# Performance work log

Measured on AMD Instinct MI355X. Metric: run time of the kernel, lower is better.

Reference implementation:

```python
import jax, jax.numpy as jnp
import numpy as np

E = 1024      # emb_size == hidden_size
H = 8         # n_heads
BATCH = 8
NUM = 48      # table rows
KW = 48       # table columns (keys)
L = NUM * KW  # 2304


def _mha(q_in, kv_in, length, Wq, bq, Wk, bk, Wv, bv, Wo, bo, n_heads=H):
    # q_in: (B, T, E), kv_in: (B, S, E); returns (T, B, E) per the torch layout.
    B, T, Em = q_in.shape
    S = kv_in.shape[1]
    dh = Em // n_heads
    q = (q_in @ Wq + bq).reshape(B, T, n_heads, dh).transpose(0, 2, 1, 3)
    k = (kv_in @ Wk + bk).reshape(B, S, n_heads, dh).transpose(0, 2, 1, 3)
    v = (kv_in @ Wv + bv).reshape(B, S, n_heads, dh).transpose(0, 2, 1, 3)
    scores = jnp.einsum('bhtd,bhsd->bhts', q, k) / jnp.asarray(np.sqrt(dh), q.dtype)
    mask = jnp.arange(S) < length  # memory_lengths masking
    scores = jnp.where(mask[None, None, None, :], scores, jnp.finfo(scores.dtype).min)
    attn = jax.nn.softmax(scores, axis=-1)
    out = jnp.einsum('bhts,bhsd->bhtd', attn, v).transpose(0, 2, 1, 3).reshape(B, T, Em)
    out = out @ Wo + bo
    return out.transpose(1, 0, 2)  # (T, B, E)


def setup_inputs() -> dict:
    key = jax.random.key(0)
    ks = jax.random.split(key, 24)

    def W(k, shape, s=0.03):
        return jax.random.normal(k, shape, dtype=jnp.float32) * s

    inp = {
        'emb': jax.random.normal(ks[0], (L, BATCH, E), dtype=jnp.float32),
        # col attention params
        'Wq_c': W(ks[1], (E, E)), 'bq_c': jnp.zeros((E,), jnp.float32),
        'Wk_c': W(ks[2], (E, E)), 'bk_c': jnp.zeros((E,), jnp.float32),
        'Wv_c': W(ks[3], (E, E)), 'bv_c': jnp.zeros((E,), jnp.float32),
        'Wo_c': W(ks[4], (E, E)), 'bo_c': jnp.zeros((E,), jnp.float32),
        # row attention params
        'Wq_r': W(ks[5], (E, E)), 'bq_r': jnp.zeros((E,), jnp.float32),
        'Wk_r': W(ks[6], (E, E)), 'bk_r': jnp.zeros((E,), jnp.float32),
        'Wv_r': W(ks[7], (E, E)), 'bv_r': jnp.zeros((E,), jnp.float32),
        'Wo_r': W(ks[8], (E, E)), 'bo_r': jnp.zeros((E,), jnp.float32),
        # fusion layers
        'W_gen': W(ks[9], (2 * E, E)),
        'W_mlp1': W(ks[10], (2 * E, E)),
        'W_mlp2': W(ks[11], (E, 1)),
        # scalar forward args
        'start_id': 0, 'end_id': L - 1,
        'num': NUM, 'num_tensor': NUM,
        'kw_num': KW, 'kw_num_tensor': KW,
        'batch': BATCH,
    }
    return inp


def reference(emb, Wq_c, bq_c, Wk_c, bk_c, Wv_c, bv_c, Wo_c, bo_c,
              Wq_r, bq_r, Wk_r, bk_r, Wv_r, bv_r, Wo_r, bo_r,
              W_gen, W_mlp1, W_mlp2,
              start_id, end_id, num, num_tensor, kw_num, kw_num_tensor, batch):
    Em = emb.shape[-1]
    length = end_id - start_id + 1  # = num * kw_num
    # emb.narrow(0, start_id, length): (L, batch, E)
    rep = emb[start_id:start_id + length]
    # -> (kw_num, batch*num, E)
    home_ply_rep = rep.transpose(1, 0, 2).reshape(batch * num, kw_num, Em).transpose(1, 0, 2)

    # --- column-dim encoding: attention over the `num` (row) axis ---
    col_mb = jnp.swapaxes(home_ply_rep.reshape(kw_num, batch, num, Em), 0, 2)  # (num, batch, kw, E)
    col_mb = col_mb.reshape(num, batch * kw_num, Em)
    col_q = col_mb.transpose(1, 0, 2)  # (batch*kw, num, E)
    col_rep = _mha(col_q, col_q, num_tensor, Wq_c, bq_c, Wk_c, bk_c, Wv_c, bv_c, Wo_c, bo_c)
    # (num, batch*kw, E) -> (kw_num, batch*num, E)
    col_dim_rep = jnp.swapaxes(col_rep.reshape(num, batch, kw_num, Em), 0, 2).reshape(kw_num, batch * num, Em)

    # --- row-dim encoding: attention over the `kw_num` (column) axis ---
    row_q = col_dim_rep.transpose(1, 0, 2)  # (batch*num, kw, E)
    row_dim_rep = _mha(row_q, row_q, kw_num_tensor, Wq_r, bq_r, Wk_r, bk_r, Wv_r, bv_r, Wo_r, bo_r)  # (kw, b*n, E)

    # --- fusion: concat + Linear + tanh, MLP scores, softmax over {row, col} ---
    gen_rep = jnp.tanh(jnp.concatenate([row_dim_rep, col_dim_rep], axis=-1) @ W_gen)

    def mlp_score(x):
        return jnp.tanh(jnp.concatenate([x, gen_rep], axis=-1) @ W_mlp1) @ W_mlp2  # (kw, b*n, 1)

    row_score = mlp_score(row_dim_rep)
    col_score = mlp_score(col_dim_rep)
    w = jax.nn.softmax(jnp.concatenate([row_score, col_score], axis=-1), axis=-1)  # (kw, b*n, 2)
    home_ply_memory_bank = w[..., 0:1] * row_dim_rep + w[..., 1:2] * col_dim_rep
    # no_fusion=True -> residual add
    home_ply_memory_bank = home_ply_memory_bank + home_ply_rep

    row_for_ptr = row_dim_rep.reshape(kw_num, batch, num, Em)
    col_for_ptr = col_dim_rep.reshape(kw_num, batch, num, Em)

    # row_aggregation == 'mean'
    home_ply_row_rep = home_ply_memory_bank.mean(axis=0)  # (batch*num, E)
    home_ply_row_rep = home_ply_row_rep.reshape(batch, num, Em).transpose(1, 0, 2)  # (num, batch, E)
    return (home_ply_row_rep, home_ply_memory_bank, col_for_ptr, row_for_ptr)
```

## Files before the change

### kernel.cpp

```cpp
#include <hip/hip_runtime.h>
#include <hip/hip_bf16.h>
#include <stdint.h>

typedef unsigned short u16;
typedef unsigned int   u32;
typedef __attribute__((ext_vector_type(4))) float f32x4;
typedef __attribute__((ext_vector_type(2))) float f32x2;
typedef __attribute__((ext_vector_type(8))) short s16x8;

#define DEV __device__ __forceinline__

static constexpr int EDIM  = 1024;
static constexpr int NB    = 48;
static constexpr int KWN   = 48;
static constexpr int BB    = 8;
static constexpr int MROWS = BB * NB * KWN;
static constexpr int MT    = MROWS / 128;

DEV float b2f(u16 x) { u32 u = ((u32)x) << 16; float f; __builtin_memcpy(&f, &u, 4); return f; }
DEV u16 f2b(float f) {
    u32 u; __builtin_memcpy(&u, &f, 4);
    u32 r = (u + 0x7FFFu + ((u >> 16) & 1u)) >> 16;
    return (u16)r;
}

#define GLDS16(gsrc, ldst) __builtin_amdgcn_global_load_lds( \
    (const __attribute__((address_space(1))) u32*)(gsrc),    \
    (__attribute__((address_space(3))) u32*)(ldst), 16, 0, 0)

__global__ void wconv_kernel(const float* __restrict__ W, u16* __restrict__ Wt,
                             int K, int N) {
    __shared__ u16 tile[64][65];
    int n0 = blockIdx.x * 64, k0 = blockIdx.y * 64;
    int tx = threadIdx.x & 63, ty = threadIdx.x >> 6;
#pragma unroll
    for (int i = 0; i < 16; ++i) {
        int r = ty * 16 + i;
        tile[r][tx] = f2b(W[(size_t)(k0 + r) * N + n0 + tx]);
    }
    __syncthreads();
#pragma unroll
    for (int i = 0; i < 16; ++i) {
        int r = ty * 16 + i;
        Wt[(size_t)(n0 + r) * K + k0 + tx] = tile[tx][r];
    }
}

__global__ void gather_kernel(const float* __restrict__ emb, u16* __restrict__ Xc) {
    int gid = blockIdx.x * 256 + threadIdx.x;
    int r = gid >> 9, c2 = gid & 511;
    int b = r / 2304, k = (r / 48) % 48, n = r % 48;
    int src = (n * 48 + k) * 8 + b;
    f32x2 v = *(const f32x2*)&emb[(size_t)src * EDIM + c2 * 2];
    u32 p = (u32)f2b(v.x) | ((u32)f2b(v.y) << 16);
    *(u32*)&Xc[(size_t)r * EDIM + c2 * 2] = p;
}

__global__ void zero_kernel(float* __restrict__ p, int n) {
    int i = blockIdx.x * 256 + threadIdx.x;
    if (i < n) p[i] = 0.f;
}

template<int KTOT, bool DUALA, bool TANH, bool PERM, bool SCORE, bool WRC>
__global__ __launch_bounds__(256, 2) void gemm_kernel(
    const u16* __restrict__ A1, const u16* __restrict__ A2,
    const u16* __restrict__ Bt, const float* __restrict__ bias,
    u16* __restrict__ C, const float* __restrict__ w2, float* __restrict__ score) {
    __shared__ u16 lA[128 * 32];
    __shared__ u16 lB[128 * 32];
    int bid = blockIdx.x;
    int mt = bid % MT, nt = bid / MT;
    int m0 = mt * 128, n0 = nt * 128;
    int tid = threadIdx.x, lane = tid & 63, wv = tid >> 6;
    int wm = wv >> 1, wn = wv & 1;
    int arow = lane >> 2, acol = (lane & 3) * 8;
    int fr = lane & 15, fk = (lane >> 4) * 8;

    f32x4 acc[4][4];
#pragma unroll
    for (int i = 0; i < 4; ++i)
#pragma unroll
        for (int j = 0; j < 4; ++j) acc[i][j] = (f32x4)0.f;

    for (int kt = 0; kt < KTOT / 32; ++kt) {
        int k0 = kt * 32;
        const u16* As = A1; int ka = k0;
        if (DUALA && k0 >= 1024) { As = A2; ka = k0 - 1024; }
        __syncthreads();
#pragma unroll
        for (int i = 0; i < 2; ++i) {
            int c = wv * 2 + i;
            const u16* ga = As + ((size_t)(m0 + c * 16 + arow) * 1024 + ka + acol);
            GLDS16(ga, &lA[c * 512]);
            const u16* gb = Bt + ((size_t)(n0 + c * 16 + arow) * KTOT + k0 + acol);
            GLDS16(gb, &lB[c * 512]);
        }
        __syncthreads();
        s16x8 af[4], bf[4];
#pragma unroll
        for (int mf = 0; mf < 4; ++mf) af[mf] = *(const s16x8*)&lA[(wm * 64 + mf * 16 + fr) * 32 + fk];
#pragma unroll
        for (int nf = 0; nf < 4; ++nf) bf[nf] = *(const s16x8*)&lB[(wn * 64 + nf * 16 + fr) * 32 + fk];
#pragma unroll
        for (int mf = 0; mf < 4; ++mf)
#pragma unroll
            for (int nf = 0; nf < 4; ++nf)
                acc[mf][nf] = __builtin_amdgcn_mfma_f32_16x16x32_bf16(af[mf], bf[nf], acc[mf][nf], 0, 0, 0);
    }

    int crow4 = (lane >> 4) * 4;
#pragma unroll
    for (int mf = 0; mf < 4; ++mf) {
#pragma unroll
        for (int j = 0; j < 4; ++j) {
            int row = m0 + wm * 64 + mf * 16 + crow4 + j;
            int orow = row;
            if (PERM) {
                int b = row / 2304, k = (row / 48) % 48, n = row % 48;
                orow = (b * 48 + n) * 48 + k;
            }
            float sc_part = 0.f;
#pragma unroll
            for (int nf = 0; nf < 4; ++nf) {
                int col = n0 + wn * 64 + nf * 16 + fr;
                float v = acc[mf][nf][j];
                if (bias) v += bias[col];
                if (TANH) v = tanhf(v);
                if (WRC) C[(size_t)orow * EDIM + col] = f2b(v);
                if (SCORE) sc_part += v * w2[col];
            }
            if (SCORE) {
                sc_part += __shfl_xor(sc_part, 1);
                sc_part += __shfl_xor(sc_part, 2);
                sc_part += __shfl_xor(sc_part, 4);
                sc_part += __shfl_xor(sc_part, 8);
                if (fr == 0) atomicAdd(&score[row], sc_part);
            }
        }
    }
}

__global__ __launch_bounds__(64) void attn_kernel(
    const u16* __restrict__ Q, const u16* __restrict__ Km,
    const u16* __restrict__ V, u16* __restrict__ O) {
    __shared__ u16 lQ[48 * 136];
    __shared__ u16 lK[48 * 136];
    __shared__ u16 lVt[128 * 72];
    __shared__ u16 lP[48 * 72];
    int bb = blockIdx.x >> 3, h = blockIdx.x & 7;
    int lane = threadIdx.x;
    size_t base = (size_t)bb * 48 * EDIM + h * 128;

#pragma unroll
    for (int i = 0; i < 48; ++i) {
        int li = i * 64 + lane;
        int row = li >> 6, c2 = li & 63;
        u32 vq = *(const u32*)&Q[base + (size_t)row * EDIM + c2 * 2];
        *(u32*)&lQ[row * 136 + c2 * 2] = vq;
        u32 vk = *(const u32*)&Km[base + (size_t)row * EDIM + c2 * 2];
        *(u32*)&lK[row * 136 + c2 * 2] = vk;
        u32 vv = *(const u32*)&V[base + (size_t)row * EDIM + c2 * 2];
        lVt[(c2 * 2) * 72 + row] = (u16)(vv & 0xffffu);
        lVt[(c2 * 2 + 1) * 72 + row] = (u16)(vv >> 16);
    }
    for (int i = lane; i < 128 * 16; i += 64) { int d = i >> 4, c = 48 + (i & 15); lVt[d * 72 + c] = 0; }
    for (int i = lane; i < 48 * 16; i += 64)  { int t = i >> 4, c = 48 + (i & 15); lP[t * 72 + c] = 0; }
    __syncthreads();

    int fr = lane & 15, fk = (lane >> 4) * 8, crow4 = (lane >> 4) * 4;
    f32x4 sc[3][3];
#pragma unroll
    for (int mf = 0; mf < 3; ++mf)
#pragma unroll
        for (int nf = 0; nf < 3; ++nf) sc[mf][nf] = (f32x4)0.f;

#pragma unroll
    for (int kk = 0; kk < 4; ++kk) {
        s16x8 aq[3], bk[3];
#pragma unroll
        for (int mf = 0; mf < 3; ++mf) aq[mf] = *(const s16x8*)&lQ[(mf * 16 + fr) * 136 + kk * 32 + fk];
#pragma unroll
        for (int nf = 0; nf < 3; ++nf) bk[nf] = *(const s16x8*)&lK[(nf * 16 + fr) * 136 + kk * 32 + fk];
#pragma unroll
        for (int mf = 0; mf < 3; ++mf)
#pragma unroll
            for (int nf = 0; nf < 3; ++nf)
                sc[mf][nf] = __builtin_amdgcn_mfma_f32_16x16x32_bf16(aq[mf], bk[nf], sc[mf][nf], 0, 0, 0);
    }

    const float scale = 0.08838834764831845f;
#pragma unroll
    for (int mf = 0; mf < 3; ++mf) {
#pragma unroll
        for (int j = 0; j < 4; ++j) {
            float v0 = sc[mf][0][j] * scale;
            float v1 = sc[mf][1][j] * scale;
            float v2 = sc[mf][2][j] * scale;
            float mx = fmaxf(v0, fmaxf(v1, v2));
            mx = fmaxf(mx, __shfl_xor(mx, 1));
            mx = fmaxf(mx, __shfl_xor(mx, 2));
            mx = fmaxf(mx, __shfl_xor(mx, 4));
            mx = fmaxf(mx, __shfl_xor(mx, 8));
            float e0 = __expf(v0 - mx), e1 = __expf(v1 - mx), e2 = __expf(v2 - mx);
            float s = e0 + e1 + e2;
            s += __shfl_xor(s, 1);
            s += __shfl_xor(s, 2);
            s += __shfl_xor(s, 4);
            s += __shfl_xor(s, 8);
            float inv = 1.f / s;
            int t = mf * 16 + crow4 + j;
            lP[t * 72 + 0  + fr] = f2b(e0 * inv);
            lP[t * 72 + 16 + fr] = f2b(e1 * inv);
            lP[t * 72 + 32 + fr] = f2b(e2 * inv);
        }
    }
    __syncthreads();

    f32x4 o[3][8];
#pragma unroll
    for (int mf = 0; mf < 3; ++mf)
#pragma unroll
        for (int nf = 0; nf < 8; ++nf) o[mf][nf] = (f32x4)0.f;

#pragma unroll
    for (int kk = 0; kk < 2; ++kk) {
        s16x8 ap[3];
#pragma unroll
        for (int mf = 0; mf < 3; ++mf) ap[mf] = *(const s16x8*)&lP[(mf * 16 + fr) * 72 + kk * 32 + fk];
#pragma unroll
        for (int nf = 0; nf < 8; ++nf) {
            s16x8 bv = *(const s16x8*)&lVt[(nf * 16 + fr) * 72 + kk * 32 + fk];
#pragma unroll
            for (int mf = 0; mf < 3; ++mf)
                o[mf][nf] = __builtin_amdgcn_mfma_f32_16x16x32_bf16(ap[mf], bv, o[mf][nf], 0, 0, 0);
        }
    }
#pragma unroll
    for (int mf = 0; mf < 3; ++mf)
#pragma unroll
        for (int nf = 0; nf < 8; ++nf)
#pragma unroll
            for (int j = 0; j < 4; ++j) {
                int t = mf * 16 + crow4 + j, d = nf * 16 + fr;
                O[base + (size_t)t * EDIM + d] = f2b(o[mf][nf][j]);
            }
}

__global__ void combine_kernel(const u16* __restrict__ RDR, const u16* __restrict__ CDR,
                               const float* __restrict__ srow, const float* __restrict__ scol,
                               const float* __restrict__ emb, float* __restrict__ out) {
    int o = blockIdx.x;
    int k = o / 384, b = (o / 48) & 7, n = o % 48;
    int r2 = (b * 48 + n) * 48 + k;
    float rs = srow[r2], cs = scol[r2];
    float m = fmaxf(rs, cs);
    float e0 = __expf(rs - m), e1 = __expf(cs - m);
    float inv = 1.f / (e0 + e1);
    float w0 = e0 * inv, w1 = e1 * inv;
    const size_t rb = (size_t)r2 * EDIM;
    const size_t ob = (size_t)o * EDIM;
    const size_t eb = ((size_t)(n * 48 + k) * 8 + b) * EDIM;
    float* out_mb  = out + 393216;
    float* out_col = out + 393216 + 18874368;
    float* out_row = out + 393216 + 2 * 18874368;
    for (int e = threadIdx.x; e < EDIM; e += 256) {
        float rv = b2f(RDR[rb + e]);
        float cv = b2f(CDR[rb + e]);
        float hv = emb[eb + e];
        out_mb[ob + e]  = w0 * rv + w1 * cv + hv;
        out_col[ob + e] = cv;
        out_row[ob + e] = rv;
    }
}

__global__ void mean_kernel(const float* __restrict__ mb, float* __restrict__ out0) {
    int idx = blockIdx.x * 256 + threadIdx.x;
    int n = idx >> 13, b = (idx >> 10) & 7, e = idx & 1023;
    float s = 0.f;
#pragma unroll 8
    for (int k = 0; k < 48; ++k) s += mb[((size_t)(k * 384 + b * 48 + n)) * EDIM + e];
    out0[idx] = s * (1.f / 48.f);
}

extern "C" void kernel_launch(void* const* d_in, const int* in_sizes, int n_in,
                              void* d_out, int out_size, void* d_ws, size_t ws_size,
                              hipStream_t stream) {
    const float* emb    = (const float*)d_in[0];
    const float* Wq_c   = (const float*)d_in[1];
    const float* bq_c   = (const float*)d_in[2];
    const float* Wk_c   = (const float*)d_in[3];
    const float* bk_c   = (const float*)d_in[4];
    const float* Wv_c   = (const float*)d_in[5];
    const float* bv_c   = (const float*)d_in[6];
    const float* Wo_c   = (const float*)d_in[7];
    const float* bo_c   = (const float*)d_in[8];
    const float* Wq_r   = (const float*)d_in[9];
    const float* bq_r   = (const float*)d_in[10];
    const float* Wk_r   = (const float*)d_in[11];
    const float* bk_r   = (const float*)d_in[12];
    const float* Wv_r   = (const float*)d_in[13];
    const float* bv_r   = (const float*)d_in[14];
    const float* Wo_r   = (const float*)d_in[15];
    const float* bo_r   = (const float*)d_in[16];
    const float* W_gen  = (const float*)d_in[17];
    const float* W_mlp1 = (const float*)d_in[18];
    const float* W_mlp2 = (const float*)d_in[19];

    char* ws = (char*)d_ws;
    const size_t WSZ = (size_t)1024 * 1024 * 2;
    u16* wt[8];
    for (int i = 0; i < 8; ++i) wt[i] = (u16*)(ws + (size_t)i * WSZ);
    u16* WgT = (u16*)(ws + 8 * WSZ);
    u16* W1T = (u16*)(ws + 10 * WSZ);
    size_t off = 12 * WSZ;
    const size_t SZ = (size_t)MROWS * EDIM * 2;
    u16* XA  = (u16*)(ws + off); off += SZ;
    u16* Qb  = (u16*)(ws + off); off += SZ;
    u16* Kb  = (u16*)(ws + off); off += SZ;
    u16* Vb  = (u16*)(ws + off); off += SZ;
    u16* CDR = (u16*)(ws + off); off += SZ;
    u16* RDR = (u16*)(ws + off); off += SZ;
    float* score_row = (float*)(ws + off); off += (size_t)MROWS * 4;
    float* score_col = (float*)(ws + off); off += (size_t)MROWS * 4;
    (void)ws_size; (void)in_sizes; (void)n_in; (void)out_size;

    dim3 tb(256);
    const float* wsrc[8] = {Wq_c, Wk_c, Wv_c, Wo_c, Wq_r, Wk_r, Wv_r, Wo_r};
    for (int i = 0; i < 8; ++i)
        wconv_kernel<<<dim3(16, 16), tb, 0, stream>>>(wsrc[i], wt[i], 1024, 1024);
    wconv_kernel<<<dim3(16, 32), tb, 0, stream>>>(W_gen, WgT, 2048, 1024);
    wconv_kernel<<<dim3(16, 32), tb, 0, stream>>>(W_mlp1, W1T, 2048, 1024);

    gather_kernel<<<MROWS * 512 / 256, tb, 0, stream>>>(emb, XA);
    zero_kernel<<<(2 * MROWS + 255) / 256, tb, 0, stream>>>(score_row, 2 * MROWS);

    const int GG = MT * 8;
    gemm_kernel<1024, false, false, false, false, true><<<GG, tb, 0, stream>>>(XA, nullptr, wt[0], bq_c, Qb, nullptr, nullptr);
    gemm_kernel<1024, false, false, false, false, true><<<GG, tb, 0, stream>>>(XA, nullptr, wt[1], bk_c, Kb, nullptr, nullptr);
    gemm_kernel<1024, false, false, false, false, true><<<GG, tb, 0, stream>>>(XA, nullptr, wt[2], bv_c, Vb, nullptr, nullptr);
    attn_kernel<<<384 * 8, 64, 0, stream>>>(Qb, Kb, Vb, XA);
    gemm_kernel<1024, false, false, true, false, true><<<GG, tb, 0, stream>>>(XA, nullptr, wt[3], bo_c, CDR, nullptr, nullptr);
    gemm_kernel<1024, false, false, false, false, true><<<GG, tb, 0, stream>>>(CDR, nullptr, wt[4], bq_r, Qb, nullptr, nullptr);
    gemm_kernel<1024, false, false, false, false, true><<<GG, tb, 0, stream>>>(CDR, nullptr, wt[5], bk_r, Kb, nullptr, nullptr);
    gemm_kernel<1024, false, false, false, false, true><<<GG, tb, 0, stream>>>(CDR, nullptr, wt[6], bv_r, Vb, nullptr, nullptr);
    attn_kernel<<<384 * 8, 64, 0, stream>>>(Qb, Kb, Vb, XA);
    gemm_kernel<1024, false, false, false, false, true><<<GG, tb, 0, stream>>>(XA, nullptr, wt[7], bo_r, RDR, nullptr, nullptr);
    gemm_kernel<2048, true, true, false, false, true><<<GG, tb, 0, stream>>>(RDR, CDR, WgT, nullptr, Qb, nullptr, nullptr);
    gemm_kernel<2048, true, true, false, true, false><<<GG, tb, 0, stream>>>(RDR, Qb, W1T, nullptr, nullptr, W_mlp2, score_row);
    gemm_kernel<2048, true, true, false, true, false><<<GG, tb, 0, stream>>>(CDR, Qb, W1T, nullptr, nullptr, W_mlp2, score_col);

    float* out = (float*)d_out;
    combine_kernel<<<MROWS, tb, 0, stream>>>(RDR, CDR, score_row, score_col, emb, out);
    mean_kernel<<<393216 / 256, tb, 0, stream>>>(out + 393216, out);
}
```

Baseline: 1.184 ms.

## Fuse QKV GEMMs, double-buffer GEMM LDS, write fp32 outputs from GEMM epilogues

Concatenates the Q/K/V weights and biases so each attention block uses one wide GEMM writing an interleaved QKV buffer. The GEMM gains double-buffered LDS staging with an XOR-style swizzle to cut bank conflicts, and raises launch bounds to 4 blocks per CU. The attention kernel reads Q and K fragments straight from global memory and writes its output in place over Q. The output-projection GEMMs write the fp32 col/row outputs directly, so the combine kernel only writes the memory bank. These changes aim to cut kernel launches, redundant A-matrix reads and memory traffic, at the cost of more LDS per block and uncoalesced direct global fragment loads in attention.

```diff
diff --git a/kernel.cpp b/kernel.cpp
--- a/kernel.cpp
+++ b/kernel.cpp
@@ -11,10 +11,7 @@
 #define DEV __device__ __forceinline__
 
 static constexpr int EDIM  = 1024;
-static constexpr int NB    = 48;
-static constexpr int KWN   = 48;
-static constexpr int BB    = 8;
-static constexpr int MROWS = BB * NB * KWN;
+static constexpr int MROWS = 8 * 48 * 48;
 static constexpr int MT    = MROWS / 128;
 
 DEV float b2f(u16 x) { u32 u = ((u32)x) << 16; float f; __builtin_memcpy(&f, &u, 4); return f; }
@@ -44,6 +41,12 @@
         int r = ty * 16 + i;
         Wt[(size_t)(n0 + r) * K + k0 + tx] = tile[tx][r];
     }
+}
+
+__global__ void bconcat_kernel(const float* __restrict__ a, const float* __restrict__ b,
+                               const float* __restrict__ c, float* __restrict__ out) {
+    int i = blockIdx.x * 256 + threadIdx.x;
+    out[i] = (i < 1024) ? a[i] : ((i < 2048) ? b[i - 1024] : c[i - 2048]);
 }
 
 __global__ void gather_kernel(const float* __restrict__ emb, u16* __restrict__ Xc) {
@@ -61,20 +64,20 @@
     if (i < n) p[i] = 0.f;
 }
 
-template<int KTOT, bool DUALA, bool TANH, bool PERM, bool SCORE, bool WRC>
-__global__ __launch_bounds__(256, 2) void gemm_kernel(
-    const u16* __restrict__ A1, const u16* __restrict__ A2,
+template<int KTOT, bool DUALA, bool TANH, bool PERM, bool SCORE, bool WRC, int OMAP>
+__global__ __launch_bounds__(256, 4) void gemm_kernel(
+    const u16* __restrict__ A1, const u16* __restrict__ A2, int lda,
     const u16* __restrict__ Bt, const float* __restrict__ bias,
-    u16* __restrict__ C, const float* __restrict__ w2, float* __restrict__ score) {
-    __shared__ u16 lA[128 * 32];
-    __shared__ u16 lB[128 * 32];
+    u16* __restrict__ C, int ldc, float* __restrict__ outF,
+    const float* __restrict__ w2, float* __restrict__ score) {
+    __shared__ u16 lA[2][128 * 32];
+    __shared__ u16 lB[2][128 * 32];
     int bid = blockIdx.x;
     int mt = bid % MT, nt = bid / MT;
     int m0 = mt * 128, n0 = nt * 128;
     int tid = threadIdx.x, lane = tid & 63, wv = tid >> 6;
     int wm = wv >> 1, wn = wv & 1;
-    int arow = lane >> 2, acol = (lane & 3) * 8;
-    int fr = lane & 15, fk = (lane >> 4) * 8;
+    int fr = lane & 15, qq = lane >> 4, fk = qq * 8;
 
     f32x4 acc[4][4];
 #pragma unroll
@@ -82,25 +85,38 @@
 #pragma unroll
         for (int j = 0; j < 4; ++j) acc[i][j] = (f32x4)0.f;
 
-    for (int kt = 0; kt < KTOT / 32; ++kt) {
+    auto STAGE = [&](int bsel, int kt) {
         int k0 = kt * 32;
         const u16* As = A1; int ka = k0;
         if (DUALA && k0 >= 1024) { As = A2; ka = k0 - 1024; }
-        __syncthreads();
 #pragma unroll
         for (int i = 0; i < 2; ++i) {
             int c = wv * 2 + i;
-            const u16* ga = As + ((size_t)(m0 + c * 16 + arow) * 1024 + ka + acol);
-            GLDS16(ga, &lA[c * 512]);
-            const u16* gb = Bt + ((size_t)(n0 + c * 16 + arow) * KTOT + k0 + acol);
-            GLDS16(gb, &lB[c * 512]);
-        }
+            int r = c * 16 + (lane >> 2);
+            int qg = ((lane & 3) - (r >> 1)) & 3;
+            GLDS16(As + (size_t)(m0 + r) * lda + ka + qg * 8, &lA[bsel][c * 512]);
+            GLDS16(Bt + (size_t)(n0 + r) * KTOT + k0 + qg * 8, &lB[bsel][c * 512]);
+        }
+    };
+
+    constexpr int NT = KTOT / 32;
+    STAGE(0, 0);
+    for (int kt = 0; kt < NT; ++kt) {
         __syncthreads();
+        if (kt + 1 < NT) STAGE((kt + 1) & 1, kt + 1);
+        const u16* la = &lA[kt & 1][0];
+        const u16* lb = &lB[kt & 1][0];
         s16x8 af[4], bf[4];
 #pragma unroll
-        for (int mf = 0; mf < 4; ++mf) af[mf] = *(const s16x8*)&lA[(wm * 64 + mf * 16 + fr) * 32 + fk];
-#pragma unroll
-        for (int nf = 0; nf < 4; ++nf) bf[nf] = *(const s16x8*)&lB[(wn * 64 + nf * 16 + fr) * 32 + fk];
+        for (int mf = 0; mf < 4; ++mf) {
+            int rr = wm * 64 + mf * 16 + fr;
+            af[mf] = *(const s16x8*)&la[rr * 32 + (((qq + (rr >> 1)) & 3) * 8)];
+        }
+#pragma unroll
+        for (int nf = 0; nf < 4; ++nf) {
+            int rn = wn * 64 + nf * 16 + fr;
+            bf[nf] = *(const s16x8*)&lb[rn * 32 + (((qq + (rn >> 1)) & 3) * 8)];
+        }
 #pragma unroll
         for (int mf = 0; mf < 4; ++mf)
 #pragma unroll
@@ -108,16 +124,22 @@
                 acc[mf][nf] = __builtin_amdgcn_mfma_f32_16x16x32_bf16(af[mf], bf[nf], acc[mf][nf], 0, 0, 0);
     }
 
-    int crow4 = (lane >> 4) * 4;
+    int crow4 = qq * 4;
 #pragma unroll
     for (int mf = 0; mf < 4; ++mf) {
 #pragma unroll
         for (int j = 0; j < 4; ++j) {
             int row = m0 + wm * 64 + mf * 16 + crow4 + j;
             int orow = row;
-            if (PERM) {
+            int o32 = 0;
+            if (PERM || OMAP == 1) {
                 int b = row / 2304, k = (row / 48) % 48, n = row % 48;
-                orow = (b * 48 + n) * 48 + k;
+                if (PERM) orow = (b * 48 + n) * 48 + k;
+                if (OMAP == 1) o32 = k * 384 + b * 48 + n;
+            }
+            if (OMAP == 2) {
+                int b = row / 2304, n = (row / 48) % 48, k = row % 48;
+                o32 = k * 384 + b * 48 + n;
             }
             float sc_part = 0.f;
 #pragma unroll
@@ -126,7 +148,8 @@
                 float v = acc[mf][nf][j];
                 if (bias) v += bias[col];
                 if (TANH) v = tanhf(v);
-                if (WRC) C[(size_t)orow * EDIM + col] = f2b(v);
+                if (WRC) C[(size_t)orow * ldc + col] = f2b(v);
+                if (OMAP) outF[(size_t)o32 * EDIM + col] = v;
                 if (SCORE) sc_part += v * w2[col];
             }
             if (SCORE) {
@@ -140,28 +163,21 @@
     }
 }
 
-__global__ __launch_bounds__(64) void attn_kernel(
-    const u16* __restrict__ Q, const u16* __restrict__ Km,
-    const u16* __restrict__ V, u16* __restrict__ O) {
-    __shared__ u16 lQ[48 * 136];
-    __shared__ u16 lK[48 * 136];
+__global__ __launch_bounds__(64) void attn_kernel(u16* __restrict__ QKV) {
     __shared__ u16 lVt[128 * 72];
     __shared__ u16 lP[48 * 72];
+    const int LDQ = 3072;
     int bb = blockIdx.x >> 3, h = blockIdx.x & 7;
     int lane = threadIdx.x;
-    size_t base = (size_t)bb * 48 * EDIM + h * 128;
+    u16* Qp = QKV + (size_t)bb * 48 * LDQ + h * 128;
+    const u16* Kp = Qp + 1024;
+    const u16* Vp = Qp + 2048;
 
 #pragma unroll
     for (int i = 0; i < 48; ++i) {
-        int li = i * 64 + lane;
-        int row = li >> 6, c2 = li & 63;
-        u32 vq = *(const u32*)&Q[base + (size_t)row * EDIM + c2 * 2];
-        *(u32*)&lQ[row * 136 + c2 * 2] = vq;
-        u32 vk = *(const u32*)&Km[base + (size_t)row * EDIM + c2 * 2];
-        *(u32*)&lK[row * 136 + c2 * 2] = vk;
-        u32 vv = *(const u32*)&V[base + (size_t)row * EDIM + c2 * 2];
-        lVt[(c2 * 2) * 72 + row] = (u16)(vv & 0xffffu);
-        lVt[(c2 * 2 + 1) * 72 + row] = (u16)(vv >> 16);
+        u32 vv = *(const u32*)&Vp[(size_t)i * LDQ + lane * 2];
+        lVt[(lane * 2) * 72 + i]     = (u16)(vv & 0xffffu);
+        lVt[(lane * 2 + 1) * 72 + i] = (u16)(vv >> 16);
     }
     for (int i = lane; i < 128 * 16; i += 64) { int d = i >> 4, c = 48 + (i & 15); lVt[d * 72 + c] = 0; }
     for (int i = lane; i < 48 * 16; i += 64)  { int t = i >> 4, c = 48 + (i & 15); lP[t * 72 + c] = 0; }
@@ -178,9 +194,9 @@
     for (int kk = 0; kk < 4; ++kk) {
         s16x8 aq[3], bk[3];
 #pragma unroll
-        for (int mf = 0; mf < 3; ++mf) aq[mf] = *(const s16x8*)&lQ[(mf * 16 + fr) * 136 + kk * 32 + fk];
-#pragma unroll
-        for (int nf = 0; nf < 3; ++nf) bk[nf] = *(const s16x8*)&lK[(nf * 16 + fr) * 136 + kk * 32 + fk];
+        for (int mf = 0; mf < 3; ++mf) aq[mf] = *(const s16x8*)&Qp[(size_t)(mf * 16 + fr) * LDQ + kk * 32 + fk];
+#pragma unroll
+        for (int nf = 0; nf < 3; ++nf) bk[nf] = *(const s16x8*)&Kp[(size_t)(nf * 16 + fr) * LDQ + kk * 32 + fk];
 #pragma unroll
         for (int mf = 0; mf < 3; ++mf)
 #pragma unroll
@@ -242,13 +258,13 @@
 #pragma unroll
             for (int j = 0; j < 4; ++j) {
                 int t = mf * 16 + crow4 + j, d = nf * 16 + fr;
-                O[base + (size_t)t * EDIM + d] = f2b(o[mf][nf][j]);
+                Qp[(size_t)t * LDQ + d] = f2b(o[mf][nf][j]);
             }
 }
 
 __global__ void combine_kernel(const u16* __restrict__ RDR, const u16* __restrict__ CDR,
                                const float* __restrict__ srow, const float* __restrict__ scol,
-                               const float* __restrict__ emb, float* __restrict__ out) {
+                               const float* __restrict__ emb, float* __restrict__ out_mb) {
     int o = blockIdx.x;
     int k = o / 384, b = (o / 48) & 7, n = o % 48;
     int r2 = (b * 48 + n) * 48 + k;
@@ -260,16 +276,10 @@
     const size_t rb = (size_t)r2 * EDIM;
     const size_t ob = (size_t)o * EDIM;
     const size_t eb = ((size_t)(n * 48 + k) * 8 + b) * EDIM;
-    float* out_mb  = out + 393216;
-    float* out_col = out + 393216 + 18874368;
-    float* out_row = out + 393216 + 2 * 18874368;
     for (int e = threadIdx.x; e < EDIM; e += 256) {
         float rv = b2f(RDR[rb + e]);
         float cv = b2f(CDR[rb + e]);
-        float hv = emb[eb + e];
-        out_mb[ob + e]  = w0 * rv + w1 * cv + hv;
-        out_col[ob + e] = cv;
-        out_row[ob + e] = rv;
+        out_mb[ob + e] = w0 * rv + w1 * cv + emb[eb + e];
     }
 }
 
@@ -307,49 +317,64 @@
     const float* W_mlp2 = (const float*)d_in[19];
 
     char* ws = (char*)d_ws;
-    const size_t WSZ = (size_t)1024 * 1024 * 2;
-    u16* wt[8];
-    for (int i = 0; i < 8; ++i) wt[i] = (u16*)(ws + (size_t)i * WSZ);
-    u16* WgT = (u16*)(ws + 8 * WSZ);
-    u16* W1T = (u16*)(ws + 10 * WSZ);
-    size_t off = 12 * WSZ;
-    const size_t SZ = (size_t)MROWS * EDIM * 2;
-    u16* XA  = (u16*)(ws + off); off += SZ;
-    u16* Qb  = (u16*)(ws + off); off += SZ;
-    u16* Kb  = (u16*)(ws + off); off += SZ;
-    u16* Vb  = (u16*)(ws + off); off += SZ;
-    u16* CDR = (u16*)(ws + off); off += SZ;
-    u16* RDR = (u16*)(ws + off); off += SZ;
-    float* score_row = (float*)(ws + off); off += (size_t)MROWS * 4;
-    float* score_col = (float*)(ws + off); off += (size_t)MROWS * 4;
+    size_t off = 0;
+    auto alloc = [&](size_t bytes) { char* p = ws + off; off += (bytes + 255) & ~(size_t)255; return p; };
+    u16*   WqkvC = (u16*)alloc((size_t)3072 * 1024 * 2);
+    u16*   WqkvR = (u16*)alloc((size_t)3072 * 1024 * 2);
+    u16*   WoC   = (u16*)alloc((size_t)1024 * 1024 * 2);
+    u16*   WoR   = (u16*)alloc((size_t)1024 * 1024 * 2);
+    u16*   WgT   = (u16*)alloc((size_t)1024 * 2048 * 2);
+    u16*   W1T   = (u16*)alloc((size_t)1024 * 2048 * 2);
+    float* bqkvC = (float*)alloc(3072 * 4);
+    float* bqkvR = (float*)alloc(3072 * 4);
+    u16*   XA    = (u16*)alloc((size_t)MROWS * 1024 * 2);
+    u16*   QKV   = (u16*)alloc((size_t)MROWS * 3072 * 2);
+    u16*   CDR   = (u16*)alloc((size_t)MROWS * 1024 * 2);
+    u16*   RDR   = (u16*)alloc((size_t)MROWS * 1024 * 2);
+    float* score_row = (float*)alloc((size_t)MROWS * 4);
+    float* score_col = (float*)alloc((size_t)MROWS * 4);
     (void)ws_size; (void)in_sizes; (void)n_in; (void)out_size;
 
     dim3 tb(256);
-    const float* wsrc[8] = {Wq_c, Wk_c, Wv_c, Wo_c, Wq_r, Wk_r, Wv_r, Wo_r};
-    for (int i = 0; i < 8; ++i)
-        wconv_kernel<<<dim3(16, 16), tb, 0, stream>>>(wsrc[i], wt[i], 1024, 1024);
-    wconv_kernel<<<dim3(16, 32), tb, 0, stream>>>(W_gen, WgT, 2048, 1024);
+    wconv_kernel<<<dim3(16, 16), tb, 0, stream>>>(Wq_c, WqkvC,                   1024, 1024);
+    wconv_kernel<<<dim3(16, 16), tb, 0, stream>>>(Wk_c, WqkvC + 1024 * 1024,     1024, 1024);
+    wconv_kernel<<<dim3(16, 16), tb, 0, stream>>>(Wv_c, WqkvC + 2 * 1024 * 1024, 1024, 1024);
+    wconv_kernel<<<dim3(16, 16), tb, 0, stream>>>(Wo_c, WoC,                     1024, 1024);
+    wconv_kernel<<<dim3(16, 16), tb, 0, stream>>>(Wq_r, WqkvR,                   1024, 1024);
+    wconv_kernel<<<dim3(16, 16), tb, 0, stream>>>(Wk_r, WqkvR + 1024 * 1024,     1024, 1024);
+    wconv_kernel<<<dim3(16, 16), tb, 0, stream>>>(Wv_r, WqkvR + 2 * 1024 * 1024, 1024, 1024);
+    wconv_kernel<<<dim3(16, 16), tb, 0, stream>>>(Wo_r, WoR,                     1024, 1024);
+    wconv_kernel<<<dim3(16, 32), tb, 0, stream>>>(W_gen,  WgT, 2048, 1024);
     wconv_kernel<<<dim3(16, 32), tb, 0, stream>>>(W_mlp1, W1T, 2048, 1024);
+    bconcat_kernel<<<12, tb, 0, stream>>>(bq_c, bk_c, bv_c, bqkvC);
+    bconcat_kernel<<<12, tb, 0, stream>>>(bq_r, bk_r, bv_r, bqkvR);
 
     gather_kernel<<<MROWS * 512 / 256, tb, 0, stream>>>(emb, XA);
     zero_kernel<<<(2 * MROWS + 255) / 256, tb, 0, stream>>>(score_row, 2 * MROWS);
 
-    const int GG = MT * 8;
-    gemm_kernel<1024, false, false, false, false, true><<<GG, tb, 0, stream>>>(XA, nullptr, wt[0], bq_c, Qb, nullptr, nullptr);
-    gemm_kernel<1024, false, false, false, false, true><<<GG, tb, 0, stream>>>(XA, nullptr, wt[1], bk_c, Kb, nullptr, nullptr);
-    gemm_kernel<1024, false, false, false, false, true><<<GG, tb, 0, stream>>>(XA, nullptr, wt[2], bv_c, Vb, nullptr, nullptr);
-    attn_kernel<<<384 * 8, 64, 0, stream>>>(Qb, Kb, Vb, XA);
-    gemm_kernel<1024, false, false, true, false, true><<<GG, tb, 0, stream>>>(XA, nullptr, wt[3], bo_c, CDR, nullptr, nullptr);
-    gemm_kernel<1024, false, false, false, false, true><<<GG, tb, 0, stream>>>(CDR, nullptr, wt[4], bq_r, Qb, nullptr, nullptr);
-    gemm_kernel<1024, false, false, false, false, true><<<GG, tb, 0, stream>>>(CDR, nullptr, wt[5], bk_r, Kb, nullptr, nullptr);
-    gemm_kernel<1024, false, false, false, false, true><<<GG, tb, 0, stream>>>(CDR, nullptr, wt[6], bv_r, Vb, nullptr, nullptr);
-    attn_kernel<<<384 * 8, 64, 0, stream>>>(Qb, Kb, Vb, XA);
-    gemm_kernel<1024, false, false, false, false, true><<<GG, tb, 0, stream>>>(XA, nullptr, wt[7], bo_r, RDR, nullptr, nullptr);
-    gemm_kernel<2048, true, true, false, false, true><<<GG, tb, 0, stream>>>(RDR, CDR, WgT, nullptr, Qb, nullptr, nullptr);
-    gemm_kernel<2048, true, true, false, true, false><<<GG, tb, 0, stream>>>(RDR, Qb, W1T, nullptr, nullptr, W_mlp2, score_row);
-    gemm_kernel<2048, true, true, false, true, false><<<GG, tb, 0, stream>>>(CDR, Qb, W1T, nullptr, nullptr, W_mlp2, score_col);
-
     float* out = (float*)d_out;
-    combine_kernel<<<MROWS, tb, 0, stream>>>(RDR, CDR, score_row, score_col, emb, out);
-    mean_kernel<<<393216 / 256, tb, 0, stream>>>(out + 393216, out);
-}
+    float* out_mb  = out + 393216;
+    float* out_col = out + 393216 + 18874368;
+    float* out_row = out + 393216 + 2 * 18874368;
+
+    const int G8 = MT * 8, G24 = MT * 24;
+    gemm_kernel<1024, false, false, false, false, true, 0><<<G24, tb, 0, stream>>>(
+        XA, nullptr, 1024, WqkvC, bqkvC, QKV, 3072, nullptr, nullptr, nullptr);
+    attn_kernel<<<384 * 8, 64, 0, stream>>>(QKV);
+    gemm_kernel<1024, false, false, true, false, true, 1><<<G8, tb, 0, stream>>>(
+        QKV, nullptr, 3072, WoC, bo_c, CDR, 1024, out_col, nullptr, nullptr);
+    gemm_kernel<1024, false, false, false, false, true, 0><<<G24, tb, 0, stream>>>(
+        CDR, nullptr, 1024, WqkvR, bqkvR, QKV, 3072, nullptr, nullptr, nullptr);
+    attn_kernel<<<384 * 8, 64, 0, stream>>>(QKV);
+    gemm_kernel<1024, false, false, false, false, true, 2><<<G8, tb, 0, stream>>>(
+        QKV, nullptr, 3072, WoR, bo_r, RDR, 1024, out_row, nullptr, nullptr);
+    gemm_kernel<2048, true, true, false, false, true, 0><<<G8, tb, 0, stream>>>(
+        RDR, CDR, 1024, WgT, nullptr, XA, 1024, nullptr, nullptr, nullptr);
+    gemm_kernel<2048, true, true, false, true, false, 0><<<G8, tb, 0, stream>>>(
+        RDR, XA, 1024, W1T, nullptr, nullptr, 1024, nullptr, W_mlp2, score_row);
+    gemm_kernel<2048, true, true, false, true, false, 0><<<G8, tb, 0, stream>>>(
+        CDR, XA, 1024, W1T, nullptr, nullptr, 1024, nullptr, W_mlp2, score_col);
+
+    combine_kernel<<<MROWS, tb, 0, stream>>>(RDR, CDR, score_row, score_col, emb, out_mb);
+    mean_kernel<<<393216 / 256, tb, 0, stream>>>(out_mb, out);
+}
```

After: 1.079 ms. 8.9% less time.
